# Performance work log

Measured on AMD Instinct MI355X. Metric: run time of the kernel, lower is better.

Reference implementation:

```python
import jax, jax.numpy as jnp
import numpy as np

B, S, DIN, DOUT = 4, 2048, 4096, 11008

def setup_inputs() -> dict:
    key = jax.random.key(0)
    k1, k2, k3 = jax.random.split(key, 3)
    x = jax.random.normal(k1, (B, S, DIN), dtype=jnp.float32)
    # int8 weight stored as int32 for portability; values in int8 range
    weight = jax.random.randint(k2, (DOUT, DIN), -127, 128, dtype=jnp.int32)
    scales = jax.random.uniform(k3, (DOUT,), dtype=jnp.float32) * 0.02 + 0.001
    return {"x": x, "weight": weight, "scales": scales}

def reference(x, weight, scales):
    # F.linear(input, weight.to(input.dtype)) * scales
    w = weight.astype(x.dtype)                      # [DOUT, DIN]
    out = jnp.einsum('bsi,oi->bso', x, w)           # [B, S, DOUT]
    return out * scales                             # per-out-channel scale
```

## Files before the change

kernel.cpp:

```cpp
#include <hip/hip_runtime.h>
#include <hip/hip_bf16.h>

#define M_DIM 8192
#define N_DIM 11008
#define K_DIM 4096

typedef __attribute__((ext_vector_type(8))) short bf16x8;
typedef __attribute__((ext_vector_type(4))) float f32x4;
typedef __attribute__((ext_vector_type(4))) int i32x4;

__device__ __forceinline__ short f2bf(float f) {
    __hip_bfloat16 h = __float2bfloat16(f);
    short s;
    __builtin_memcpy(&s, &h, sizeof(s));
    return s;
}

__device__ __forceinline__ void gload_lds16(const void* g, void* l) {
    __builtin_amdgcn_global_load_lds(
        (const __attribute__((address_space(1))) unsigned int*)g,
        (__attribute__((address_space(3))) unsigned int*)l, 16, 0, 0);
}

#define MFMAI8(A, Bv, C) __builtin_amdgcn_mfma_i32_16x16x64_i8((A), (Bv), (C), 0, 0, 0)
#define MFMA16(A, Bv, C) __builtin_amdgcn_mfma_f32_16x16x32_bf16((A), (Bv), (C), 0, 0, 0)


__global__ __launch_bounds__(256)
void quant_x_i8(const float* __restrict__ X, char* __restrict__ Xq,
                float* __restrict__ RS) {
    const int row  = blockIdx.x * 4 + (threadIdx.x >> 6);
    const int lane = threadIdx.x & 63;
    const float* xr = X + (size_t)row * K_DIM;

    float4 v[16];
    float am = 0.0f;
    #pragma unroll
    for (int c = 0; c < 16; ++c) {
        v[c] = *reinterpret_cast<const float4*>(xr + c * 256 + lane * 4);
        am = fmaxf(am, fmaxf(fmaxf(fabsf(v[c].x), fabsf(v[c].y)),
                             fmaxf(fabsf(v[c].z), fabsf(v[c].w))));
    }
    #pragma unroll
    for (int off = 1; off < 64; off <<= 1)
        am = fmaxf(am, __shfl_xor(am, off));

    const float inv = 127.0f / am;
    int* xq32 = reinterpret_cast<int*>(Xq + (size_t)row * K_DIM);
    #pragma unroll
    for (int c = 0; c < 16; ++c) {
        int c0 = __float2int_rn(v[c].x * inv);
        int c1 = __float2int_rn(v[c].y * inv);
        int c2 = __float2int_rn(v[c].z * inv);
        int c3 = __float2int_rn(v[c].w * inv);
        xq32[c * 64 + lane] = (c0 & 255) | ((c1 & 255) << 8) |
                              ((c2 & 255) << 16) | (c3 << 24);
    }
    if (lane == 0) RS[row] = am / 127.0f;
}


__global__ __launch_bounds__(256)
void cvt_w_i8(const int* __restrict__ W, char* __restrict__ Wq, int n16) {
    int i = blockIdx.x * blockDim.x + threadIdx.x;
    const int stride = gridDim.x * blockDim.x;
    for (; i < n16; i += stride) {
        const int4* p = reinterpret_cast<const int4*>(W + (size_t)i * 16);
        int4 a = p[0], b = p[1], c = p[2], d = p[3];
        int4 o;
        o.x = (a.x & 255) | ((a.y & 255) << 8) | ((a.z & 255) << 16) | (a.w << 24);
        o.y = (b.x & 255) | ((b.y & 255) << 8) | ((b.z & 255) << 16) | (b.w << 24);
        o.z = (c.x & 255) | ((c.y & 255) << 8) | ((c.z & 255) << 16) | (c.w << 24);
        o.w = (d.x & 255) | ((d.y & 255) << 8) | ((d.z & 255) << 16) | (d.w << 24);
        *reinterpret_cast<int4*>(Wq + (size_t)i * 16) = o;
    }
}


#define STA(T, B, H) do { \
    const char* s_ = gA + (size_t)((H) * 128) * K_DIM + (T) * 128; \
    char* d_ = As + (B) * 32768 + (H) * 16384 + aw; \
    gload_lds16(s_, d_); \
    gload_lds16(s_ + (size_t)64 * K_DIM, d_ + 8192); \
} while (0)

#define STB(T, B, H) do { \
    const char* s_ = gB + (size_t)((H) * 128) * K_DIM + (T) * 128; \
    char* d_ = Bs + (B) * 32768 + (H) * 16384 + aw; \
    gload_lds16(s_, d_); \
    gload_lds16(s_ + (size_t)64 * K_DIM, d_ + 8192); \
} while (0)

#define TILE_BODY(T, B, MODE) do { \
    const char* Ab_ = As + (B) * 32768; \
    const char* Bb_ = Bs + (B) * 32768; \
    i32x4 a0_[4][2], a1_[4][2], b0_[2][2], b1_[2][2]; \
    _Pragma("unroll") for (int m = 0; m < 4; ++m) { \
        a0_[m][0] = *(const i32x4*)(Ab_ + fa + m * 2048 + cs0); \
        a0_[m][1] = *(const i32x4*)(Ab_ + fa + m * 2048 + cs1); } \
    _Pragma("unroll") for (int n = 0; n < 2; ++n) { \
        b0_[n][0] = *(const i32x4*)(Bb_ + fb + n * 2048 + cs0); \
        b0_[n][1] = *(const i32x4*)(Bb_ + fb + n * 2048 + cs1); } \
    if ((MODE) < 2) STA((T) + 1, 1 - (B), 0); \
    __builtin_amdgcn_s_barrier(); \
    asm volatile("s_waitcnt lgkmcnt(0)" ::: "memory"); \
    __builtin_amdgcn_s_setprio(1); \
    _Pragma("unroll") for (int m = 0; m < 4; ++m) \
    _Pragma("unroll") for (int n = 0; n < 2; ++n) { \
        acc[m][n] = MFMAI8(a0_[m][0], b0_[n][0], acc[m][n]); \
        acc[m][n] = MFMAI8(a0_[m][1], b0_[n][1], acc[m][n]); } \
    __builtin_amdgcn_s_setprio(0); \
    __builtin_amdgcn_s_barrier(); \
    _Pragma("unroll") for (int n = 0; n < 2; ++n) { \
        b1_[n][0] = *(const i32x4*)(Bb_ + fb + (n + 2) * 2048 + cs0); \
        b1_[n][1] = *(const i32x4*)(Bb_ + fb + (n + 2) * 2048 + cs1); } \
    if ((MODE) < 2) STA((T) + 1, 1 - (B), 1); \
    __builtin_amdgcn_s_barrier(); \
    asm volatile("s_waitcnt lgkmcnt(0)" ::: "memory"); \
    __builtin_amdgcn_s_setprio(1); \
    _Pragma("unroll") for (int m = 0; m < 4; ++m) \
    _Pragma("unroll") for (int n = 0; n < 2; ++n) { \
        acc[m][n + 2] = MFMAI8(a0_[m][0], b1_[n][0], acc[m][n + 2]); \
        acc[m][n + 2] = MFMAI8(a0_[m][1], b1_[n][1], acc[m][n + 2]); } \
    __builtin_amdgcn_s_setprio(0); \
    __builtin_amdgcn_s_barrier(); \
    _Pragma("unroll") for (int m = 0; m < 4; ++m) { \
        a1_[m][0] = *(const i32x4*)(Ab_ + fa + (m + 4) * 2048 + cs0); \
        a1_[m][1] = *(const i32x4*)(Ab_ + fa + (m + 4) * 2048 + cs1); } \
    if ((MODE) == 0) STB((T) + 2, (B), 0); \
    __builtin_amdgcn_s_barrier(); \
    asm volatile("s_waitcnt lgkmcnt(0)" ::: "memory"); \
    __builtin_amdgcn_s_setprio(1); \
    _Pragma("unroll") for (int m = 0; m < 4; ++m) \
    _Pragma("unroll") for (int n = 0; n < 2; ++n) { \
        acc[m + 4][n] = MFMAI8(a1_[m][0], b0_[n][0], acc[m + 4][n]); \
        acc[m + 4][n] = MFMAI8(a1_[m][1], b0_[n][1], acc[m + 4][n]); } \
    __builtin_amdgcn_s_setprio(0); \
    __builtin_amdgcn_s_barrier(); \
    if ((MODE) == 0) STB((T) + 2, (B), 1); \
    __builtin_amdgcn_s_setprio(1); \
    _Pragma("unroll") for (int m = 0; m < 4; ++m) \
    _Pragma("unroll") for (int n = 0; n < 2; ++n) { \
        acc[m + 4][n + 2] = MFMAI8(a1_[m][0], b1_[n][0], acc[m + 4][n + 2]); \
        acc[m + 4][n + 2] = MFMAI8(a1_[m][1], b1_[n][1], acc[m + 4][n + 2]); } \
    __builtin_amdgcn_s_setprio(0); \
    if ((MODE) == 0) asm volatile("s_waitcnt vmcnt(4)" ::: "memory"); \
    if ((MODE) == 1) asm volatile("s_waitcnt vmcnt(0)" ::: "memory"); \
    __builtin_amdgcn_s_barrier(); \
} while (0)

__global__ __launch_bounds__(512, 2)
void gemm_i8(const char* __restrict__ Xq, const char* __restrict__ Wq,
             const float* __restrict__ RS, const float* __restrict__ SC,
             float* __restrict__ Out)
{
    __shared__ __attribute__((aligned(16))) char smem[131072];
    char* const As = smem;
    char* const Bs = smem + 65536;

    const int tid  = threadIdx.x;
    const int lane = tid & 63;
    const int w    = tid >> 6;
    const int wr   = w >> 2;
    const int wc   = w & 3;

    const int wg  = blockIdx.x;
    const int swz = (wg & 7) * 172 + (wg >> 3);
    const int by  = swz / 43;
    const int bx  = swz - by * 43;
    const int brow = by * 256;
    const int bcol = bx * 256;

    const int lr = lane >> 3;
    const int lc = (lane & 7) ^ lr;
    const char* gA = Xq + (size_t)(brow + w * 8 + lr) * K_DIM + (lc << 4);
    const char* gB = Wq + (size_t)(bcol + w * 8 + lr) * K_DIM + (lc << 4);
    const int aw = w * 1024;

    const int fa  = (wr * 128 + (lane & 15)) * 128;
    const int fb  = (wc * 64  + (lane & 15)) * 128;
    const int cs0 = (((lane >> 4) + 0) ^ (lane & 7)) * 16;
    const int cs1 = (((lane >> 4) + 4) ^ (lane & 7)) * 16;

    i32x4 acc[8][4] = {};

    STB(0, 0, 0); STB(0, 0, 1); STA(0, 0, 0); STA(0, 0, 1);
    STB(1, 1, 0); STB(1, 1, 1);
    asm volatile("s_waitcnt vmcnt(4)" ::: "memory");
    __builtin_amdgcn_s_barrier();

    for (int t = 0; t < 30; t += 2) {
        TILE_BODY(t, 0, 0);
        TILE_BODY(t + 1, 1, 0);
    }
    TILE_BODY(30, 0, 1);
    TILE_BODY(31, 1, 2);

    const int orow0 = brow + wr * 128 + ((lane >> 4) << 2);
    const int ocol0 = bcol + wc * 64 + (lane & 15);
    float rsv[8][4];
    #pragma unroll
    for (int m = 0; m < 8; ++m)
        #pragma unroll
        for (int j = 0; j < 4; ++j)
            rsv[m][j] = RS[orow0 + m * 16 + j];
    #pragma unroll
    for (int n = 0; n < 4; ++n) {
        const float sc = SC[ocol0 + n * 16];
        #pragma unroll
        for (int m = 0; m < 8; ++m)
            #pragma unroll
            for (int j = 0; j < 4; ++j)
                __builtin_nontemporal_store(
                    (float)acc[m][n][j] * (rsv[m][j] * sc),
                    &Out[(size_t)(orow0 + m * 16 + j) * N_DIM + (ocol0 + n * 16)]);
    }
}


__global__ __launch_bounds__(256, 2)
void wo_int8_gemm_fused(const float* __restrict__ X, const int* __restrict__ W,
                        const float* __restrict__ SC, float* __restrict__ Out)
{
    __shared__ short Asf[128 * 64];
    __shared__ short Bsf[128 * 64];

    const int tid  = threadIdx.x;
    const int lane = tid & 63;
    const int wid  = tid >> 6;
    const int wrf  = wid >> 1;
    const int wcf  = wid & 1;
    const int brow = blockIdx.y * 128;
    const int bcol = blockIdx.x * 128;
    const int srow = tid >> 3;
    const int scol = (tid & 7) << 3;
    const int arow   = wrf * 64 + (lane & 15);
    const int brow_f = wcf * 64 + (lane & 15);
    const int koff   = (lane >> 4) << 3;

    f32x4 acc[4][4] = {};

    for (int k0 = 0; k0 < K_DIM; k0 += 64) {
        __syncthreads();
        #pragma unroll
        for (int p = 0; p < 4; ++p) {
            const int r = p * 32 + srow;
            const float4* xs = reinterpret_cast<const float4*>(
                X + (size_t)(brow + r) * K_DIM + (k0 + scol));
            float4 a0 = xs[0], a1 = xs[1];
            bf16x8 v;
            v[0] = f2bf(a0.x); v[1] = f2bf(a0.y); v[2] = f2bf(a0.z); v[3] = f2bf(a0.w);
            v[4] = f2bf(a1.x); v[5] = f2bf(a1.y); v[6] = f2bf(a1.z); v[7] = f2bf(a1.w);
            *reinterpret_cast<bf16x8*>(&Asf[(r * 64 + scol) ^ ((r & 7) << 3)]) = v;
        }
        #pragma unroll
        for (int p = 0; p < 4; ++p) {
            const int r = p * 32 + srow;
            const int4* ws = reinterpret_cast<const int4*>(
                W + (size_t)(bcol + r) * K_DIM + (k0 + scol));
            int4 b0 = ws[0], b1 = ws[1];
            bf16x8 v;
            v[0] = f2bf((float)b0.x); v[1] = f2bf((float)b0.y);
            v[2] = f2bf((float)b0.z); v[3] = f2bf((float)b0.w);
            v[4] = f2bf((float)b1.x); v[5] = f2bf((float)b1.y);
            v[6] = f2bf((float)b1.z); v[7] = f2bf((float)b1.w);
            *reinterpret_cast<bf16x8*>(&Bsf[(r * 64 + scol) ^ ((r & 7) << 3)]) = v;
        }
        __syncthreads();
        #pragma unroll
        for (int ks = 0; ks < 2; ++ks) {
            const int kb = ks * 32 + koff;
            bf16x8 af[4], bfr[4];
            #pragma unroll
            for (int m = 0; m < 4; ++m) {
                const int r = arow + m * 16;
                af[m] = *reinterpret_cast<const bf16x8*>(&Asf[(r * 64 + kb) ^ ((r & 7) << 3)]);
            }
            #pragma unroll
            for (int n = 0; n < 4; ++n) {
                const int r = brow_f + n * 16;
                bfr[n] = *reinterpret_cast<const bf16x8*>(&Bsf[(r * 64 + kb) ^ ((r & 7) << 3)]);
            }
            #pragma unroll
            for (int m = 0; m < 4; ++m)
                #pragma unroll
                for (int n = 0; n < 4; ++n)
                    acc[m][n] = MFMA16(af[m], bfr[n], acc[m][n]);
        }
    }

    const int orow0 = brow + wrf * 64 + ((lane >> 4) << 2);
    const int ocol0 = bcol + wcf * 64 + (lane & 15);
    #pragma unroll
    for (int n = 0; n < 4; ++n) {
        const float sc = SC[ocol0 + n * 16];
        #pragma unroll
        for (int m = 0; m < 4; ++m)
            #pragma unroll
            for (int j = 0; j < 4; ++j)
                Out[(size_t)(orow0 + m * 16 + j) * N_DIM + (ocol0 + n * 16)]
                    = acc[m][n][j] * sc;
    }
}

extern "C" void kernel_launch(void* const* d_in, const int* in_sizes, int n_in,
                              void* d_out, int out_size, void* d_ws, size_t ws_size,
                              hipStream_t stream) {
    const float* X  = (const float*)d_in[0];
    const int*   W  = (const int*)d_in[1];
    const float* SC = (const float*)d_in[2];
    float* Out = (float*)d_out;

    const size_t xq_bytes = (size_t)M_DIM * K_DIM;
    const size_t wq_bytes = (size_t)N_DIM * K_DIM;
    const size_t rs_bytes = (size_t)M_DIM * sizeof(float);
    if (ws_size >= xq_bytes + wq_bytes + rs_bytes) {
        char*  Xq = (char*)d_ws;
        char*  Wq = (char*)d_ws + xq_bytes;
        float* RS = (float*)((char*)d_ws + xq_bytes + wq_bytes);
        quant_x_i8<<<M_DIM / 4, 256, 0, stream>>>(X, Xq, RS);
        cvt_w_i8<<<2048, 256, 0, stream>>>(W, Wq, (int)((size_t)N_DIM * K_DIM / 16));
        gemm_i8<<<(M_DIM / 256) * (N_DIM / 256), 512, 0, stream>>>(Xq, Wq, RS, SC, Out);
    } else {
        dim3 grid(N_DIM / 128, M_DIM / 128);
        wo_int8_gemm_fused<<<grid, 256, 0, stream>>>(X, W, SC, Out);
    }
}
```

Before: 429.8 us.

## Split the int8 GEMM 256x256 tile across 16 waves with fewer barriers

The int8 MFMA GEMM now launches 1024 threads per block instead of 512. Each wave computes a 64x64 sub-tile instead of 128x64, so each thread holds half as many accumulators and issues one global-to-LDS load per stage half instead of two. The per-tile schedule is rearranged to follow the two K-halves (cs0 then cs1) rather than M and N quadrants, and it drops one barrier and LDS wait phase per tile. The row-scale epilogue now uses vector loads. The stricter launch bound (1024, 4) may force a very low VGPR budget and cause spills, and the single resident block per CU depends on more barriers across more waves.

After: 444.4 us. 1.03x slower.

```diff
diff --git a/kernel.cpp b/kernel.cpp
--- a/kernel.cpp
+++ b/kernel.cpp
@@ -77,82 +77,62 @@
 }
 
 
-#define STA(T, B, H) do { \
-    const char* s_ = gA + (size_t)((H) * 128) * K_DIM + (T) * 128; \
-    char* d_ = As + (B) * 32768 + (H) * 16384 + aw; \
-    gload_lds16(s_, d_); \
-    gload_lds16(s_ + (size_t)64 * K_DIM, d_ + 8192); \
-} while (0)
-
-#define STB(T, B, H) do { \
-    const char* s_ = gB + (size_t)((H) * 128) * K_DIM + (T) * 128; \
-    char* d_ = Bs + (B) * 32768 + (H) * 16384 + aw; \
-    gload_lds16(s_, d_); \
-    gload_lds16(s_ + (size_t)64 * K_DIM, d_ + 8192); \
-} while (0)
+#define STA(T, B, H) \
+    gload_lds16(gA + (size_t)((H) * 128) * K_DIM + (T) * 128, \
+                As + (B) * 32768 + (H) * 16384 + aw)
+
+#define STB(T, B, H) \
+    gload_lds16(gB + (size_t)((H) * 128) * K_DIM + (T) * 128, \
+                Bs + (B) * 32768 + (H) * 16384 + aw)
 
 #define TILE_BODY(T, B, MODE) do { \
     const char* Ab_ = As + (B) * 32768; \
     const char* Bb_ = Bs + (B) * 32768; \
-    i32x4 a0_[4][2], a1_[4][2], b0_[2][2], b1_[2][2]; \
-    _Pragma("unroll") for (int m = 0; m < 4; ++m) { \
-        a0_[m][0] = *(const i32x4*)(Ab_ + fa + m * 2048 + cs0); \
-        a0_[m][1] = *(const i32x4*)(Ab_ + fa + m * 2048 + cs1); } \
-    _Pragma("unroll") for (int n = 0; n < 2; ++n) { \
-        b0_[n][0] = *(const i32x4*)(Bb_ + fb + n * 2048 + cs0); \
-        b0_[n][1] = *(const i32x4*)(Bb_ + fb + n * 2048 + cs1); } \
+    i32x4 a0_[4], b0_[4], a1_[4], b1_[4]; \
+     \
+    _Pragma("unroll") for (int m = 0; m < 4; ++m) \
+        a0_[m] = *(const i32x4*)(Ab_ + fa + m * 2048 + cs0); \
+    _Pragma("unroll") for (int n = 0; n < 4; ++n) \
+        b0_[n] = *(const i32x4*)(Bb_ + fb + n * 2048 + cs0); \
     if ((MODE) < 2) STA((T) + 1, 1 - (B), 0); \
     __builtin_amdgcn_s_barrier(); \
     asm volatile("s_waitcnt lgkmcnt(0)" ::: "memory"); \
     __builtin_amdgcn_s_setprio(1); \
     _Pragma("unroll") for (int m = 0; m < 4; ++m) \
-    _Pragma("unroll") for (int n = 0; n < 2; ++n) { \
-        acc[m][n] = MFMAI8(a0_[m][0], b0_[n][0], acc[m][n]); \
-        acc[m][n] = MFMAI8(a0_[m][1], b0_[n][1], acc[m][n]); } \
+    _Pragma("unroll") for (int n = 0; n < 4; ++n) \
+        acc[m][n] = MFMAI8(a0_[m], b0_[n], acc[m][n]); \
     __builtin_amdgcn_s_setprio(0); \
     __builtin_amdgcn_s_barrier(); \
-    _Pragma("unroll") for (int n = 0; n < 2; ++n) { \
-        b1_[n][0] = *(const i32x4*)(Bb_ + fb + (n + 2) * 2048 + cs0); \
-        b1_[n][1] = *(const i32x4*)(Bb_ + fb + (n + 2) * 2048 + cs1); } \
+     \
+    _Pragma("unroll") for (int m = 0; m < 4; ++m) \
+        a1_[m] = *(const i32x4*)(Ab_ + fa + m * 2048 + cs1); \
+    _Pragma("unroll") for (int n = 0; n < 4; ++n) \
+        b1_[n] = *(const i32x4*)(Bb_ + fb + n * 2048 + cs1); \
     if ((MODE) < 2) STA((T) + 1, 1 - (B), 1); \
     __builtin_amdgcn_s_barrier(); \
     asm volatile("s_waitcnt lgkmcnt(0)" ::: "memory"); \
     __builtin_amdgcn_s_setprio(1); \
-    _Pragma("unroll") for (int m = 0; m < 4; ++m) \
-    _Pragma("unroll") for (int n = 0; n < 2; ++n) { \
-        acc[m][n + 2] = MFMAI8(a0_[m][0], b1_[n][0], acc[m][n + 2]); \
-        acc[m][n + 2] = MFMAI8(a0_[m][1], b1_[n][1], acc[m][n + 2]); } \
+    _Pragma("unroll") for (int m = 0; m < 2; ++m) \
+    _Pragma("unroll") for (int n = 0; n < 4; ++n) \
+        acc[m][n] = MFMAI8(a1_[m], b1_[n], acc[m][n]); \
     __builtin_amdgcn_s_setprio(0); \
     __builtin_amdgcn_s_barrier(); \
-    _Pragma("unroll") for (int m = 0; m < 4; ++m) { \
-        a1_[m][0] = *(const i32x4*)(Ab_ + fa + (m + 4) * 2048 + cs0); \
-        a1_[m][1] = *(const i32x4*)(Ab_ + fa + (m + 4) * 2048 + cs1); } \
-    if ((MODE) == 0) STB((T) + 2, (B), 0); \
-    __builtin_amdgcn_s_barrier(); \
-    asm volatile("s_waitcnt lgkmcnt(0)" ::: "memory"); \
+     \
+    if ((MODE) == 0) { STB((T) + 2, (B), 0); STB((T) + 2, (B), 1); } \
     __builtin_amdgcn_s_setprio(1); \
-    _Pragma("unroll") for (int m = 0; m < 4; ++m) \
-    _Pragma("unroll") for (int n = 0; n < 2; ++n) { \
-        acc[m + 4][n] = MFMAI8(a1_[m][0], b0_[n][0], acc[m + 4][n]); \
-        acc[m + 4][n] = MFMAI8(a1_[m][1], b0_[n][1], acc[m + 4][n]); } \
+    _Pragma("unroll") for (int m = 2; m < 4; ++m) \
+    _Pragma("unroll") for (int n = 0; n < 4; ++n) \
+        acc[m][n] = MFMAI8(a1_[m], b1_[n], acc[m][n]); \
     __builtin_amdgcn_s_setprio(0); \
-    __builtin_amdgcn_s_barrier(); \
-    if ((MODE) == 0) STB((T) + 2, (B), 1); \
-    __builtin_amdgcn_s_setprio(1); \
-    _Pragma("unroll") for (int m = 0; m < 4; ++m) \
-    _Pragma("unroll") for (int n = 0; n < 2; ++n) { \
-        acc[m + 4][n + 2] = MFMAI8(a1_[m][0], b1_[n][0], acc[m + 4][n + 2]); \
-        acc[m + 4][n + 2] = MFMAI8(a1_[m][1], b1_[n][1], acc[m + 4][n + 2]); } \
-    __builtin_amdgcn_s_setprio(0); \
-    if ((MODE) == 0) asm volatile("s_waitcnt vmcnt(4)" ::: "memory"); \
+    if ((MODE) == 0) asm volatile("s_waitcnt vmcnt(2)" ::: "memory"); \
     if ((MODE) == 1) asm volatile("s_waitcnt vmcnt(0)" ::: "memory"); \
-    __builtin_amdgcn_s_barrier(); \
+    if ((MODE) < 2) __builtin_amdgcn_s_barrier(); \
 } while (0)
 
-__global__ __launch_bounds__(512, 2)
-void gemm_i8(const char* __restrict__ Xq, const char* __restrict__ Wq,
-             const float* __restrict__ RS, const float* __restrict__ SC,
-             float* __restrict__ Out)
+__global__ __launch_bounds__(1024, 4)
+void gemm_i8_hw(const char* __restrict__ Xq, const char* __restrict__ Wq,
+                const float* __restrict__ RS, const float* __restrict__ SC,
+                float* __restrict__ Out)
 {
     __shared__ __attribute__((aligned(16))) char smem[131072];
     char* const As = smem;
@@ -177,16 +157,16 @@
     const char* gB = Wq + (size_t)(bcol + w * 8 + lr) * K_DIM + (lc << 4);
     const int aw = w * 1024;
 
-    const int fa  = (wr * 128 + (lane & 15)) * 128;
-    const int fb  = (wc * 64  + (lane & 15)) * 128;
+    const int fa  = (wr * 64 + (lane & 15)) * 128;
+    const int fb  = (wc * 64 + (lane & 15)) * 128;
     const int cs0 = (((lane >> 4) + 0) ^ (lane & 7)) * 16;
     const int cs1 = (((lane >> 4) + 4) ^ (lane & 7)) * 16;
 
-    i32x4 acc[8][4] = {};
+    i32x4 acc[4][4] = {};
 
     STB(0, 0, 0); STB(0, 0, 1); STA(0, 0, 0); STA(0, 0, 1);
     STB(1, 1, 0); STB(1, 1, 1);
-    asm volatile("s_waitcnt vmcnt(4)" ::: "memory");
+    asm volatile("s_waitcnt vmcnt(2)" ::: "memory");
     __builtin_amdgcn_s_barrier();
 
     for (int t = 0; t < 30; t += 2) {
@@ -196,19 +176,17 @@
     TILE_BODY(30, 0, 1);
     TILE_BODY(31, 1, 2);
 
-    const int orow0 = brow + wr * 128 + ((lane >> 4) << 2);
+    const int orow0 = brow + wr * 64 + ((lane >> 4) << 2);
     const int ocol0 = bcol + wc * 64 + (lane & 15);
-    float rsv[8][4];
-    #pragma unroll
-    for (int m = 0; m < 8; ++m)
-        #pragma unroll
-        for (int j = 0; j < 4; ++j)
-            rsv[m][j] = RS[orow0 + m * 16 + j];
+    f32x4 rsv[4];
+    #pragma unroll
+    for (int m = 0; m < 4; ++m)
+        rsv[m] = *reinterpret_cast<const f32x4*>(&RS[orow0 + m * 16]);
     #pragma unroll
     for (int n = 0; n < 4; ++n) {
         const float sc = SC[ocol0 + n * 16];
         #pragma unroll
-        for (int m = 0; m < 8; ++m)
+        for (int m = 0; m < 4; ++m)
             #pragma unroll
             for (int j = 0; j < 4; ++j)
                 __builtin_nontemporal_store(
@@ -320,7 +298,7 @@
         float* RS = (float*)((char*)d_ws + xq_bytes + wq_bytes);
         quant_x_i8<<<M_DIM / 4, 256, 0, stream>>>(X, Xq, RS);
         cvt_w_i8<<<2048, 256, 0, stream>>>(W, Wq, (int)((size_t)N_DIM * K_DIM / 16));
-        gemm_i8<<<(M_DIM / 256) * (N_DIM / 256), 512, 0, stream>>>(Xq, Wq, RS, SC, Out);
+        gemm_i8_hw<<<(M_DIM / 256) * (N_DIM / 256), 1024, 0, stream>>>(Xq, Wq, RS, SC, Out);
     } else {
         dim3 grid(N_DIM / 128, M_DIM / 128);
         wo_int8_gemm_fused<<<grid, 256, 0, stream>>>(X, W, SC, Out);
```
